# Optimization experiments

Measured on AMD Instinct MI355X. Metric: run time of the kernel, lower is better.

## Reference

```python
import jax, jax.numpy as jnp
import numpy as np

N_NODES = 100000
N_EDGES = 3200000
IN_DIM = 128
HID_DIM = 128
N_LAYERS = 3


def setup_inputs() -> dict:
    key = jax.random.key(0)
    ks = jax.random.split(key, 3 + 2 * N_LAYERS)
    inp = {
        "feats": jax.random.normal(ks[0], (N_NODES, IN_DIM), dtype=jnp.float32),
        "edge_src": jax.random.randint(ks[1], (N_EDGES,), 0, N_NODES, dtype=jnp.int32),
        "edge_dst": jax.random.randint(ks[2], (N_EDGES,), 0, N_NODES, dtype=jnp.int32),
    }
    d_in = IN_DIM
    for l in range(N_LAYERS):
        scale = 1.0 / np.sqrt(d_in)
        inp[f"W{l}"] = jax.random.uniform(ks[3 + 2 * l], (d_in, HID_DIM), jnp.float32, -scale, scale)
        inp[f"b{l}"] = jax.random.uniform(ks[4 + 2 * l], (HID_DIM,), jnp.float32, -scale, scale)
        inp[f"eps{l}"] = jnp.zeros((), jnp.float32)  # learn_eps init 0
        d_in = HID_DIM
    return inp


def _gin_layer(h, src, dst, W, b, eps):
    # sum aggregation over in-neighbors: agg[i] = sum_{(s->i)} h[s]
    agg = jax.ops.segment_sum(h[src], dst, num_segments=N_NODES)
    return ((1.0 + eps) * h + agg) @ W + b


def reference(feats, edge_src, edge_dst, W0, b0, eps0, W1, b1, eps1, W2, b2, eps2):
    h = feats
    for W, b, eps in ((W0, b0, eps0), (W1, b1, eps1), (W2, b2, eps2)):
        h = _gin_layer(h, edge_src, edge_dst, W, b, eps)
        # dropout is identity at p=0 / eval
    return h
```

## Files before the change

### kernel.cpp

```cpp
#include <hip/hip_runtime.h>

#define N_NODES 100000
#define N_EDGES 3200000
#define DIM 128
#define GROWS (N_NODES + 1)
#define NBUCK 391
#define NBP 392
#define EB_BLOCKS 782
#define BSLACK 2048
#define MAXPAD 9984


__device__ __forceinline__ unsigned rne_bf16(float f) {
    unsigned u = __builtin_bit_cast(unsigned, f);
    return (u + 0x7FFFu + ((u >> 16) & 1u)) >> 16;
}
__device__ __forceinline__ float bf16lo(unsigned u) {
    return __builtin_bit_cast(float, u << 16);
}
__device__ __forceinline__ float bf16hi(unsigned u) {
    return __builtin_bit_cast(float, u & 0xFFFF0000u);
}


__global__ __launch_bounds__(256) void bhist_k(const int* __restrict__ dst,
                                               int* __restrict__ bucketTotal,
                                               int* __restrict__ bhArr) {
    __shared__ int h[NBP];
    int tid = threadIdx.x;
    for (int i = tid; i < NBP; i += 256) h[i] = 0;
    __syncthreads();
#pragma unroll
    for (int c = 0; c < 4; c++) {
        int e = blockIdx.x * 4096 + c * 1024 + tid * 4;
        if (e < N_EDGES) {
            int4 d4 = ((const int4*)dst)[e >> 2];
            atomicAdd(&h[d4.x >> 8], 1);
            atomicAdd(&h[d4.y >> 8], 1);
            atomicAdd(&h[d4.z >> 8], 1);
            atomicAdd(&h[d4.w >> 8], 1);
        }
    }
    __syncthreads();
    for (int i = tid; i < NBP; i += 256) {
        int v = h[i];
        bhArr[blockIdx.x * NBP + i] = v;
        if (v > 0) atomicAdd(&bucketTotal[i], v);
    }
}

__global__ __launch_bounds__(512) void bscan_k(const int* __restrict__ bucketTotal,
                                               int* __restrict__ bucketBase,
                                               int* __restrict__ bucketCursor) {
    __shared__ int tmp[512];
    int tid = threadIdx.x;
    int v = (tid < NBP) ? bucketTotal[tid] : 0;
    tmp[tid] = v;
    __syncthreads();
    for (int off = 1; off < 512; off <<= 1) {
        int x = tmp[tid];
        if (tid >= off) x += tmp[tid - off];
        __syncthreads();
        tmp[tid] = x;
        __syncthreads();
    }
    if (tid < NBP) {
        int excl = tmp[tid] - v;
        bucketBase[tid] = excl;
        bucketCursor[tid] = excl;
        if (tid == NBP - 1) bucketBase[NBP] = tmp[tid];
    }
}

__global__ __launch_bounds__(512) void bscatter_k(const int* __restrict__ src,
                                                  const int* __restrict__ dst,
                                                  const int* __restrict__ bhArr,
                                                  int* __restrict__ bucketCursor,
                                                  int* __restrict__ ebuf) {
    __shared__ int lcur0[NBP];
    __shared__ int pexc[NBP];
    __shared__ int lofs[NBP];
    __shared__ int pfx[512];
    __shared__ int sortedv[4096];
    __shared__ int gaddr[4096];
    int tid = threadIdx.x;
    int bid = blockIdx.x;
    int v = 0;
    if (tid < NBP) {
        v = bhArr[bid * NBP + tid];
        lcur0[tid] = (v > 0) ? atomicAdd(&bucketCursor[tid], v) : 0;
    }
    pfx[tid] = v;
    __syncthreads();
    for (int off = 1; off < 512; off <<= 1) {
        int x = pfx[tid];
        if (tid >= off) x += pfx[tid - off];
        __syncthreads();
        pfx[tid] = x;
        __syncthreads();
    }
    if (tid < NBP) {
        int ex = pfx[tid] - v;
        pexc[tid] = ex;
        lofs[tid] = ex;
    }
    __syncthreads();
#pragma unroll
    for (int c = 0; c < 2; c++) {
        int e = bid * 4096 + c * 2048 + tid * 4;
        if (e < N_EDGES) {
            int4 d4 = ((const int4*)dst)[e >> 2];
            int4 s4 = ((const int4*)src)[e >> 2];
            int b0 = d4.x >> 8, b1 = d4.y >> 8, b2 = d4.z >> 8, b3 = d4.w >> 8;
            int t0 = atomicAdd(&lofs[b0], 1);
            int t1 = atomicAdd(&lofs[b1], 1);
            int t2 = atomicAdd(&lofs[b2], 1);
            int t3 = atomicAdd(&lofs[b3], 1);
            sortedv[t0] = (s4.x << 8) | (d4.x & 255);
            sortedv[t1] = (s4.y << 8) | (d4.y & 255);
            sortedv[t2] = (s4.z << 8) | (d4.z & 255);
            sortedv[t3] = (s4.w << 8) | (d4.w & 255);
            gaddr[t0] = lcur0[b0] + (t0 - pexc[b0]);
            gaddr[t1] = lcur0[b1] + (t1 - pexc[b1]);
            gaddr[t2] = lcur0[b2] + (t2 - pexc[b2]);
            gaddr[t3] = lcur0[b3] + (t3 - pexc[b3]);
        }
    }
    __syncthreads();
    int totalE = min(4096, N_EDGES - bid * 4096);
    for (int j = tid; j < totalE; j += 512)
        ebuf[gaddr[j]] = sortedv[j];
}

__global__ __launch_bounds__(256) void bfinal_k(const int* __restrict__ ebuf,
                                                const int* __restrict__ bucketBase,
                                                int* __restrict__ offsets,
                                                int* __restrict__ nbArr,
                                                int* __restrict__ csr) {
    __shared__ int srt[MAXPAD];
    __shared__ int cnt[256];
    __shared__ int sc[256];
    __shared__ int cur[256];
    int tid = threadIdx.x;
    int b = blockIdx.x;
    int s = bucketBase[b], e = bucketBase[b + 1];
    int m = e - s;
    cnt[tid] = 0;
    __syncthreads();
    for (int i = tid; i < m; i += 256)
        atomicAdd(&cnt[ebuf[s + i] & 255], 1);
    __syncthreads();
    int c = cnt[tid];
    int pad = (c + 3) & ~3;
    sc[tid] = pad;
    __syncthreads();
    for (int off = 1; off < 256; off <<= 1) {
        int x = sc[tid];
        if (tid >= off) x += sc[tid - off];
        __syncthreads();
        sc[tid] = x;
        __syncthreads();
    }
    int pexcl = sc[tid] - pad;
    int gbase = s + b * BSLACK;
    int node = b * 256 + tid;
    if (node < N_NODES) {
        offsets[node] = gbase + pexcl;
        nbArr[node] = pad >> 2;
    }
    cur[tid] = pexcl;
    __syncthreads();
    int padTot = sc[255];
    if (padTot <= MAXPAD) {
        for (int j = tid; j < padTot; j += 256) srt[j] = N_NODES;
        __syncthreads();
        for (int i = tid; i < m; i += 256) {
            int pk = ebuf[s + i];
            int pos = atomicAdd(&cur[pk & 255], 1);
            srt[pos] = (int)((unsigned)pk >> 8);
        }
        __syncthreads();
        for (int j = tid; j < padTot; j += 256)
            csr[gbase + j] = srt[j];
    } else {
        for (int i = tid; i < m; i += 256) {
            int pk = ebuf[s + i];
            int pos = atomicAdd(&cur[pk & 255], 1);
            csr[gbase + pos] = (int)((unsigned)pk >> 8);
        }
        __syncthreads();
        int pend = pexcl + pad;
        for (int p2 = cur[tid]; p2 < pend; p2++) csr[gbase + p2] = N_NODES;
    }
}


__global__ __launch_bounds__(256) void gemm_k(const float* __restrict__ H,
                                              const float* __restrict__ W,
                                              unsigned short* __restrict__ G) {
    __shared__ float hs[64][128];
    int tid = threadIdx.x;
    int rowBase = blockIdx.x * 64;
    for (int i = tid; i < 64 * 32; i += 256) {
        int r = i >> 5, c4 = i & 31;
        int row = rowBase + r;
        float4 v = make_float4(0.f, 0.f, 0.f, 0.f);
        if (row < N_NODES) v = ((const float4*)(H + (size_t)row * DIM))[c4];
        ((float4*)&hs[r][0])[c4] = v;
    }
    __syncthreads();

    int tx = tid & 31, ty = tid >> 5;
    int c0 = tx * 4, r0 = ty * 8;
    float4 acc[8];
#pragma unroll
    for (int r = 0; r < 8; r++) acc[r] = make_float4(0.f, 0.f, 0.f, 0.f);

#pragma unroll 4
    for (int k = 0; k < DIM; k++) {
        float4 wv = *(const float4*)(W + (size_t)k * DIM + c0);
#pragma unroll
        for (int r = 0; r < 8; r++) {
            float a = hs[r0 + r][k];
            acc[r].x += a * wv.x;
            acc[r].y += a * wv.y;
            acc[r].z += a * wv.z;
            acc[r].w += a * wv.w;
        }
    }
#pragma unroll
    for (int r = 0; r < 8; r++) {
        int row = rowBase + r0 + r;
        if (row <= N_NODES) {
            uint2 pk;
            pk.x = rne_bf16(acc[r].x) | (rne_bf16(acc[r].y) << 16);
            pk.y = rne_bf16(acc[r].z) | (rne_bf16(acc[r].w) << 16);
            *(uint2*)(G + (size_t)row * DIM + c0) = pk;
        }
    }
}

__device__ __forceinline__ void accum8(float* acc, uint4 v) {
    acc[0] += bf16lo(v.x); acc[1] += bf16hi(v.x);
    acc[2] += bf16lo(v.y); acc[3] += bf16hi(v.y);
    acc[4] += bf16lo(v.z); acc[5] += bf16hi(v.z);
    acc[6] += bf16lo(v.w); acc[7] += bf16hi(v.w);
}

__global__ __launch_bounds__(256) void agg_k(const unsigned short* __restrict__ G,
                                             const int* __restrict__ off,
                                             const int* __restrict__ nbArr,
                                             const int* __restrict__ csr,
                                             const float* __restrict__ bias,
                                             const float* __restrict__ epsp,
                                             float* __restrict__ out) {
    int tid = threadIdx.x;
    int lane = tid & 63;
    int node = blockIdx.x * 4 + (tid >> 6);
    int quarter = lane >> 4;
    int q = lane & 15;
    float e1 = 1.0f + epsp[0];

    int offA = off[node];
    int nb = nbArr[node];
    const int* clb = csr + offA + quarter;

    float acc[8] = {0.f, 0.f, 0.f, 0.f, 0.f, 0.f, 0.f, 0.f};

    int b = 0;
    for (; b + 4 <= nb; b += 4) {
        int i0 = clb[0];
        int i1 = clb[4];
        int i2 = clb[8];
        int i3 = clb[12];
        clb += 16;
        uint4 g0 = *(const uint4*)(G + (size_t)i0 * DIM + q * 8);
        uint4 g1 = *(const uint4*)(G + (size_t)i1 * DIM + q * 8);
        uint4 g2 = *(const uint4*)(G + (size_t)i2 * DIM + q * 8);
        uint4 g3 = *(const uint4*)(G + (size_t)i3 * DIM + q * 8);
        accum8(acc, g0);
        accum8(acc, g1);
        accum8(acc, g2);
        accum8(acc, g3);
    }
    for (; b < nb; b++) {
        int i0 = clb[0];
        clb += 4;
        uint4 g0 = *(const uint4*)(G + (size_t)i0 * DIM + q * 8);
        accum8(acc, g0);
    }

#pragma unroll
    for (int j = 0; j < 8; j++) {
        acc[j] += __shfl_xor(acc[j], 16);
        acc[j] += __shfl_xor(acc[j], 32);
    }

    if (quarter == 0) {
        uint4 sv = *(const uint4*)(G + (size_t)node * DIM + q * 8);
        float4 b0 = *(const float4*)(bias + q * 8);
        float4 b1 = *(const float4*)(bias + q * 8 + 4);
        float* op = out + (size_t)node * DIM + q * 8;
        float4 r0, r1;
        r0.x = acc[0] + e1 * bf16lo(sv.x) + b0.x;
        r0.y = acc[1] + e1 * bf16hi(sv.x) + b0.y;
        r0.z = acc[2] + e1 * bf16lo(sv.y) + b0.z;
        r0.w = acc[3] + e1 * bf16hi(sv.y) + b0.w;
        r1.x = acc[4] + e1 * bf16lo(sv.z) + b1.x;
        r1.y = acc[5] + e1 * bf16hi(sv.z) + b1.y;
        r1.z = acc[6] + e1 * bf16lo(sv.w) + b1.z;
        r1.w = acc[7] + e1 * bf16hi(sv.w) + b1.w;
        *(float4*)op = r0;
        *(float4*)(op + 4) = r1;
    }
}


extern "C" void kernel_launch(void* const* d_in, const int* in_sizes, int n_in,
                              void* d_out, int out_size, void* d_ws, size_t ws_size,
                              hipStream_t stream) {
    const float* feats = (const float*)d_in[0];
    const int* esrc = (const int*)d_in[1];
    const int* edst = (const int*)d_in[2];
    const float* Wm[3] = {(const float*)d_in[3], (const float*)d_in[6], (const float*)d_in[9]};
    const float* Bv[3] = {(const float*)d_in[4], (const float*)d_in[7], (const float*)d_in[10]};
    const float* Ev[3] = {(const float*)d_in[5], (const float*)d_in[8], (const float*)d_in[11]};
    float* out = (float*)d_out;

    char* ws = (char*)d_ws;
    unsigned short* bufG = (unsigned short*)(ws);
    int* ebuf       = (int*)(ws + 25600512);
    int* csr        = (int*)(ws + 38400512);
    int* offsets    = (int*)(ws + 54411776);
    int* nbArr      = (int*)(ws + 54811776);
    int* bucketTotal= (int*)(ws + 55211776);
    int* bucketBase = (int*)(ws + 55213376);
    int* bucketCur  = (int*)(ws + 55215040);
    int* bhArr      = (int*)(ws + 55216640);

    hipMemsetAsync(bucketTotal, 0, NBP * sizeof(int), stream);
    bhist_k<<<EB_BLOCKS, 256, 0, stream>>>(edst, bucketTotal, bhArr);
    bscan_k<<<1, 512, 0, stream>>>(bucketTotal, bucketBase, bucketCur);
    bscatter_k<<<EB_BLOCKS, 512, 0, stream>>>(esrc, edst, bhArr, bucketCur, ebuf);
    bfinal_k<<<NBUCK, 256, 0, stream>>>(ebuf, bucketBase, offsets, nbArr, csr);

    const float* h = feats;
    for (int l = 0; l < 3; l++) {
        gemm_k<<<(N_NODES + 64) / 64, 256, 0, stream>>>(h, Wm[l], bufG);
        agg_k<<<N_NODES / 4, 256, 0, stream>>>(bufG, offsets, nbArr, csr, Bv[l], Ev[l], out);
        h = out;
    }
}
```

Measured before the change: 673.8 us.

## Use split-bf16 MFMA for the dense layer GEMM with prepacked weights

Replaces the fp32 shared-memory FMA GEMM with one built on bf16 MFMA 16x16x32 instructions. Each operand is split into a high and a low bf16 part and three products are summed, to keep accuracy close to fp32. A new prep kernel splits and packs each layer's weights into fragment order once per call, and the GEMM reads H rows directly into registers with no LDS staging. The cost is three MFMAs per tile, three extra small launches, and narrow 2-byte scattered stores of the G output.

```diff
diff --git a/kernel.cpp b/kernel.cpp
--- a/kernel.cpp
+++ b/kernel.cpp
@@ -10,6 +10,9 @@
 #define BSLACK 2048
 #define MAXPAD 9984
 
+typedef __attribute__((ext_vector_type(8))) short short8;
+typedef __attribute__((ext_vector_type(4))) float f32x4;
+
 
 __device__ __forceinline__ unsigned rne_bf16(float f) {
     unsigned u = __builtin_bit_cast(unsigned, f);
@@ -20,6 +23,11 @@
 }
 __device__ __forceinline__ float bf16hi(unsigned u) {
     return __builtin_bit_cast(float, u & 0xFFFF0000u);
+}
+__device__ __forceinline__ void split2(float x, unsigned short& h, unsigned short& l) {
+    unsigned hu = rne_bf16(x);
+    h = (unsigned short)hu;
+    l = (unsigned short)rne_bf16(x - bf16lo(hu));
 }
 
 
@@ -195,47 +203,80 @@
 }
 
 
+__global__ __launch_bounds__(64) void prepw_k(const float* __restrict__ W,
+                                              unsigned short* __restrict__ Wh,
+                                              unsigned short* __restrict__ Wl) {
+    int l = threadIdx.x;
+    int t = blockIdx.x;
+    int col = ((t >> 2) << 4) + (l & 15);
+    int k0 = ((t & 3) << 5) + ((l >> 4) << 3);
+    unsigned hw[4], lw[4];
+#pragma unroll
+    for (int p = 0; p < 4; p++) {
+        float x0 = W[(size_t)(k0 + 2 * p) * DIM + col];
+        float x1 = W[(size_t)(k0 + 2 * p + 1) * DIM + col];
+        unsigned short h0, l0, h1, l1;
+        split2(x0, h0, l0);
+        split2(x1, h1, l1);
+        hw[p] = (unsigned)h0 | ((unsigned)h1 << 16);
+        lw[p] = (unsigned)l0 | ((unsigned)l1 << 16);
+    }
+    size_t base = ((size_t)t * 64 + l) * 8;
+    *(uint4*)(Wh + base) = make_uint4(hw[0], hw[1], hw[2], hw[3]);
+    *(uint4*)(Wl + base) = make_uint4(lw[0], lw[1], lw[2], lw[3]);
+}
+
 __global__ __launch_bounds__(256) void gemm_k(const float* __restrict__ H,
-                                              const float* __restrict__ W,
+                                              const unsigned short* __restrict__ Wh,
+                                              const unsigned short* __restrict__ Wl,
                                               unsigned short* __restrict__ G) {
-    __shared__ float hs[64][128];
-    int tid = threadIdx.x;
-    int rowBase = blockIdx.x * 64;
-    for (int i = tid; i < 64 * 32; i += 256) {
-        int r = i >> 5, c4 = i & 31;
-        int row = rowBase + r;
-        float4 v = make_float4(0.f, 0.f, 0.f, 0.f);
-        if (row < N_NODES) v = ((const float4*)(H + (size_t)row * DIM))[c4];
-        ((float4*)&hs[r][0])[c4] = v;
-    }
-    __syncthreads();
-
-    int tx = tid & 31, ty = tid >> 5;
-    int c0 = tx * 4, r0 = ty * 8;
-    float4 acc[8];
-#pragma unroll
-    for (int r = 0; r < 8; r++) acc[r] = make_float4(0.f, 0.f, 0.f, 0.f);
-
-#pragma unroll 4
-    for (int k = 0; k < DIM; k++) {
-        float4 wv = *(const float4*)(W + (size_t)k * DIM + c0);
-#pragma unroll
-        for (int r = 0; r < 8; r++) {
-            float a = hs[r0 + r][k];
-            acc[r].x += a * wv.x;
-            acc[r].y += a * wv.y;
-            acc[r].z += a * wv.z;
-            acc[r].w += a * wv.w;
-        }
-    }
-#pragma unroll
-    for (int r = 0; r < 8; r++) {
-        int row = rowBase + r0 + r;
-        if (row <= N_NODES) {
-            uint2 pk;
-            pk.x = rne_bf16(acc[r].x) | (rne_bf16(acc[r].y) << 16);
-            pk.y = rne_bf16(acc[r].z) | (rne_bf16(acc[r].w) << 16);
-            *(uint2*)(G + (size_t)row * DIM + c0) = pk;
+    int tid = threadIdx.x;
+    int l = tid & 63;
+    int wv = tid >> 6;
+    int rowBase = blockIdx.x * 64 + wv * 16;
+    int r = rowBase + (l & 15);
+    int kg = (l >> 4) << 3;
+    const float* hp = H + (size_t)((r < N_NODES) ? r : 0) * DIM;
+    float zmask = (r < N_NODES) ? 1.0f : 0.0f;
+
+    f32x4 acc[8];
+#pragma unroll
+    for (int cb = 0; cb < 8; cb++) acc[cb] = (f32x4){0.f, 0.f, 0.f, 0.f};
+
+#pragma unroll
+    for (int ks = 0; ks < 4; ks++) {
+        float4 u0 = *(const float4*)(hp + ks * 32 + kg);
+        float4 u1 = *(const float4*)(hp + ks * 32 + kg + 4);
+        short8 ah, al;
+        unsigned short hh, ll;
+        split2(u0.x * zmask, hh, ll); ah[0] = hh; al[0] = ll;
+        split2(u0.y * zmask, hh, ll); ah[1] = hh; al[1] = ll;
+        split2(u0.z * zmask, hh, ll); ah[2] = hh; al[2] = ll;
+        split2(u0.w * zmask, hh, ll); ah[3] = hh; al[3] = ll;
+        split2(u1.x * zmask, hh, ll); ah[4] = hh; al[4] = ll;
+        split2(u1.y * zmask, hh, ll); ah[5] = hh; al[5] = ll;
+        split2(u1.z * zmask, hh, ll); ah[6] = hh; al[6] = ll;
+        split2(u1.w * zmask, hh, ll); ah[7] = hh; al[7] = ll;
+#pragma unroll
+        for (int cb = 0; cb < 8; cb++) {
+            size_t fidx = (size_t)((cb * 4 + ks) * 64 + l) * 8;
+            short8 bh = *(const short8*)(Wh + fidx);
+            short8 bl = *(const short8*)(Wl + fidx);
+            acc[cb] = __builtin_amdgcn_mfma_f32_16x16x32_bf16(ah, bh, acc[cb], 0, 0, 0);
+            acc[cb] = __builtin_amdgcn_mfma_f32_16x16x32_bf16(al, bh, acc[cb], 0, 0, 0);
+            acc[cb] = __builtin_amdgcn_mfma_f32_16x16x32_bf16(ah, bl, acc[cb], 0, 0, 0);
+        }
+    }
+
+    int ro = rowBase + ((l >> 4) << 2);
+    int co = l & 15;
+#pragma unroll
+    for (int cb = 0; cb < 8; cb++) {
+#pragma unroll
+        for (int j = 0; j < 4; j++) {
+            int rr = ro + j;
+            if (rr <= N_NODES)
+                G[(size_t)rr * DIM + cb * 16 + co] = (unsigned short)rne_bf16(acc[cb][j]);
         }
     }
 }
@@ -337,6 +378,10 @@
     int* bucketBase = (int*)(ws + 55213376);
     int* bucketCur  = (int*)(ws + 55215040);
     int* bhArr      = (int*)(ws + 55216640);
+    unsigned short* wfrag = (unsigned short*)(ws + 56442816);
+
+    for (int l = 0; l < 3; l++)
+        prepw_k<<<32, 64, 0, stream>>>(Wm[l], wfrag + l * 32768, wfrag + l * 32768 + 16384);
 
     hipMemsetAsync(bucketTotal, 0, NBP * sizeof(int), stream);
     bhist_k<<<EB_BLOCKS, 256, 0, stream>>>(edst, bucketTotal, bhArr);
@@ -346,7 +391,8 @@
 
     const float* h = feats;
     for (int l = 0; l < 3; l++) {
-        gemm_k<<<(N_NODES + 64) / 64, 256, 0, stream>>>(h, Wm[l], bufG);
+        gemm_k<<<(N_NODES + 63) / 64, 256, 0, stream>>>(h, wfrag + l * 32768,
+                                                        wfrag + l * 32768 + 16384, bufG);
         agg_k<<<N_NODES / 4, 256, 0, stream>>>(bufG, offsets, nbArr, csr, Bv[l], Ev[l], out);
         h = out;
     }
```

Measured after the change: 595.6 us. 11.6% less time.
